# Optimization experiments

Hardware: AMD Instinct MI355X
Metric: run time of the kernel (lower is better)

## Reference

```python
import jax, jax.numpy as jnp
import numpy as np

WINDOW = 512
OVERLAP = 64
STRIDE = WINDOW - OVERLAP  # 448
HEADS = 12
HEAD_DIM = 3072 // HEADS  # 256
SCALE = 1.0 / np.sqrt(HEAD_DIM)


def setup_inputs() -> dict:
    key = jax.random.key(0)
    ks = jax.random.split(key, 9)
    B, S, H = 1, 8192, 3072
    w = 0.02  # weight init scale
    return {
        "hidden_states": jax.random.normal(ks[0], (B, S, H), jnp.float32),
        "Wq": jax.random.normal(ks[1], (H, H), jnp.float32) * w,
        "bq": jnp.zeros((H,), jnp.float32),
        "Wk": jax.random.normal(ks[2], (H, H), jnp.float32) * w,
        "bk": jnp.zeros((H,), jnp.float32),
        "Wv": jax.random.normal(ks[3], (H, H), jnp.float32) * w,
        "bv": jnp.zeros((H,), jnp.float32),
        "Wo": jax.random.normal(ks[4], (H, H), jnp.float32) * w,
        "bo": jnp.zeros((H,), jnp.float32),
    }


def reference(hidden_states, Wq, bq, Wk, bk, Wv, bv, Wo, bo):
    B, S, H = hidden_states.shape
    n_win = -(-S // STRIDE)  # ceil: windows start at 0, STRIDE, 2*STRIDE, ... < S
    starts = np.arange(n_win) * STRIDE                      # static
    idx = starts[:, None] + np.arange(WINDOW)[None, :]      # [n_win, W]
    valid = jnp.asarray(idx < S)                            # [n_win, W] bool
    idx_c = np.minimum(idx, S - 1)                          # clamp for gather

    # Gather overlapping windows: [B, n_win, W, H] (redundant QKV on overlap, as in original)
    win = hidden_states[:, idx_c]

    def proj(Wm, bm):
        y = jnp.einsum('bnwh,oh->bnwo', win, Wm) + bm
        return y.reshape(B, n_win, WINDOW, HEADS, HEAD_DIM)

    q = proj(Wq, bq)
    k = proj(Wk, bk)
    v = proj(Wv, bv)

    scores = jnp.einsum('bnqhd,bnkhd->bnhqk', q, k) * SCALE  # [B,n_win,heads,W,W]
    # Padded (out-of-range) key positions of the short last window must not attend
    scores = jnp.where(valid[None, :, None, None, :], scores, -1e9)
    attn = jax.nn.softmax(scores, axis=-1)
    ctx = jnp.einsum('bnhqk,bnkhd->bnqhd', attn, v)
    ctx = ctx.reshape(B, n_win, WINDOW, H)
    out_w = jnp.einsum('bnwh,oh->bnwo', ctx, Wo) + bo        # [B,n_win,W,H]

    # zero padded query rows, then overlap-add + average
    out_w = out_w * valid[None, :, :, None].astype(out_w.dtype)
    flat_idx = jnp.asarray(idx_c.reshape(-1))                # [n_win*W]
    output = jnp.zeros((B, S, H), out_w.dtype).at[:, flat_idx].add(
        out_w.reshape(B, -1, H))
    counts = jnp.zeros((S,), out_w.dtype).at[flat_idx].add(
        valid.reshape(-1).astype(out_w.dtype))
    return output / jnp.maximum(counts, 1.0)[None, :, None]
```

## Files before the change

kernel.cpp:

```cpp
#include <hip/hip_runtime.h>
#include <hip/hip_bf16.h>
#include <stdint.h>

#define SEQ   8192
#define HDIM  3072
#define NWIN  19
#define WINL  512
#define STR   448
#define NHEAD 12
#define DHEAD 256
#define QKVN  9216
#define ATTN_SCALE 0.0625f

typedef unsigned short u16;
typedef __bf16 bf16x8 __attribute__((ext_vector_type(8)));
typedef float  f32x4  __attribute__((ext_vector_type(4)));
typedef unsigned short us8 __attribute__((ext_vector_type(8)));

__device__ __forceinline__ u16 f2b(float x) {
  return __builtin_bit_cast(u16, __float2bfloat16(x));
}
__device__ __forceinline__ float b2f(u16 u) {
  return __builtin_bit_cast(float, (unsigned int)(u) << 16);
}
__device__ __forceinline__ void gload_lds16(const void* g, void* l) {
  __builtin_amdgcn_global_load_lds(
      (const __attribute__((address_space(1))) void*)g,
      (__attribute__((address_space(3))) void*)l, 16, 0, 0);
}

__global__ __launch_bounds__(256) void cvt_f32_bf16(const float* __restrict__ src,
                                                    u16* __restrict__ dst, int n8) {
  int i = blockIdx.x * 256 + threadIdx.x;
  if (i >= n8) return;
  const float4* s4 = (const float4*)src;
  float4 a = s4[2 * i], b = s4[2 * i + 1];
  us8 o;
  o[0] = f2b(a.x); o[1] = f2b(a.y); o[2] = f2b(a.z); o[3] = f2b(a.w);
  o[4] = f2b(b.x); o[5] = f2b(b.y); o[6] = f2b(b.z); o[7] = f2b(b.w);
  *((us8*)dst + i) = o;
}

__global__ __launch_bounds__(256) void biascat(const float* __restrict__ bq,
                                               const float* __restrict__ bk,
                                               const float* __restrict__ bv,
                                               float* __restrict__ dst) {
  int i = blockIdx.x * 256 + threadIdx.x;
  if (i >= QKVN) return;
  dst[i] = (i < HDIM) ? bq[i] : ((i < 2 * HDIM) ? bk[i - HDIM] : bv[i - 2 * HDIM]);
}

template <bool BF16OUT>
__global__ __launch_bounds__(512, 2) void gemm256(const u16* __restrict__ A,
                                                  const u16* __restrict__ B,
                                                  const float* __restrict__ bias,
                                                  float* __restrict__ outF,
                                                  u16* __restrict__ outB,
                                                  int M, int N, int K, int nbn) {
  __shared__ __align__(16) u16 As[4][4096];
  __shared__ __align__(16) u16 Bs[4][4096];
  const int tid = threadIdx.x;
  const int w = tid >> 6, l = tid & 63;
  const int wm = w >> 2, wn = w & 3;
  const int fr = l & 15, g = l >> 4;
  const int nwg = gridDim.x;
  const int bid = blockIdx.x;
  const int wg = (bid & 7) * (nwg >> 3) + (bid >> 3);
  const int bm = wg / nbn, bn = wg % nbn;

  const u16* Ab = A + (size_t)bm * 256 * K;
  const u16* Bb = B + (size_t)bn * 256 * K;

  const int r_st = w * 16 + (l >> 2);
  const int s_st = ((l & 3) ^ ((l >> 3) & 3)) * 8;
  const int sw = (g ^ ((fr >> 1) & 3)) * 8;

  f32x4 acc[8][4];
#pragma unroll
  for (int i = 0; i < 8; ++i)
#pragma unroll
    for (int j = 0; j < 4; ++j) acc[i][j] = (f32x4){0.f, 0.f, 0.f, 0.f};

  auto stA = [&](int U, int h) {
    gload_lds16(Ab + (size_t)(h * 128 + r_st) * K + U * 32 + s_st,
                (char*)&As[(2 * U + h) & 3][0] + w * 1024);
  };
  auto stB = [&](int U, int h) {
    gload_lds16(Bb + (size_t)(h * 128 + r_st) * K + U * 32 + s_st,
                (char*)&Bs[(2 * U + h) & 3][0] + w * 1024);
  };

  stA(0, 0); stA(0, 1); stB(0, 0); stB(0, 1); stA(1, 0); stA(1, 1);
  asm volatile("s_waitcnt vmcnt(2)" ::: "memory");
  __builtin_amdgcn_s_barrier();
  __builtin_amdgcn_sched_barrier(0);

  const int NT = K >> 5;

  auto step = [&](int T, bool doB, bool doA, int vm) {
    const u16* ap = &As[(2 * T + wm) & 3][0] + fr * 32 + sw;
    const u16* bp = &Bs[(2 * T + (wn >> 1)) & 3][0] + (wn & 1) * 64 * 32 + fr * 32 + sw;
    bf16x8 af[8], bf[4];
#pragma unroll
    for (int mi = 0; mi < 8; ++mi) af[mi] = *(const bf16x8*)(ap + mi * 512);
#pragma unroll
    for (int ni = 0; ni < 4; ++ni) bf[ni] = *(const bf16x8*)(bp + ni * 512);
    if (doB) { stB(T + 1, 0); stB(T + 1, 1); }
    __builtin_amdgcn_s_barrier();
    __builtin_amdgcn_s_setprio(1);
#pragma unroll
    for (int mi = 0; mi < 4; ++mi)
#pragma unroll
      for (int ni = 0; ni < 4; ++ni)
        acc[mi][ni] = __builtin_amdgcn_mfma_f32_16x16x32_bf16(af[mi], bf[ni], acc[mi][ni], 0, 0, 0);
    __builtin_amdgcn_s_setprio(0);
    __builtin_amdgcn_s_barrier();
    if (doA) { stA(T + 2, 0); stA(T + 2, 1); }
    __builtin_amdgcn_s_barrier();
    __builtin_amdgcn_s_setprio(1);
#pragma unroll
    for (int mi = 4; mi < 8; ++mi)
#pragma unroll
      for (int ni = 0; ni < 4; ++ni)
        acc[mi][ni] = __builtin_amdgcn_mfma_f32_16x16x32_bf16(af[mi], bf[ni], acc[mi][ni], 0, 0, 0);
    __builtin_amdgcn_s_setprio(0);
    if (vm == 2) asm volatile("s_waitcnt vmcnt(2)" ::: "memory");
    else if (vm == 0) asm volatile("s_waitcnt vmcnt(0)" ::: "memory");
    __builtin_amdgcn_s_barrier();
    __builtin_amdgcn_sched_barrier(0);
  };

#pragma unroll 2
  for (int T = 0; T < NT - 2; ++T) step(T, true, true, 2);
  step(NT - 2, true, false, 0);
  step(NT - 1, false, false, -1);

#pragma unroll
  for (int ni = 0; ni < 4; ++ni) {
    const int c = bn * 256 + wn * 64 + ni * 16 + fr;
    const float bvv = bias ? bias[c] : 0.0f;
#pragma unroll
    for (int mi = 0; mi < 8; ++mi) {
      const int r0 = bm * 256 + wm * 128 + mi * 16 + g * 4;
#pragma unroll
      for (int jj = 0; jj < 4; ++jj) {
        float v = acc[mi][ni][jj] + bvv;
        if (BF16OUT) outB[(size_t)(r0 + jj) * N + c] = f2b(v);
        else         outF[(size_t)(r0 + jj) * N + c] = v;
      }
    }
  }
}

__global__ __launch_bounds__(256) void vtrans(const u16* __restrict__ QKV,
                                              u16* __restrict__ Vt) {
  __shared__ u16 t[64][72];
  const int tid = threadIdx.x;
  const int s0 = blockIdx.x * 64, c0 = blockIdx.y * 64;
  {
    const int r2 = tid >> 3, cc = (tid & 7) * 8;
#pragma unroll
    for (int p = 0; p < 2; ++p) {
      const int row = r2 + p * 32;
      u16 tmp[8];
      *(uint4*)tmp = *(const uint4*)(QKV + (size_t)(s0 + row) * QKVN + 2 * HDIM + c0 + cc);
#pragma unroll
      for (int j = 0; j < 8; ++j) t[row][cc + j] = tmp[j];
    }
  }
  __syncthreads();
  {
    const int cr2 = tid >> 3, sc = tid & 7;
#pragma unroll
    for (int p = 0; p < 2; ++p) {
      const int c = cr2 + p * 32;
      u16 tmp[8];
#pragma unroll
      for (int j = 0; j < 8; ++j) tmp[j] = t[sc * 8 + j][c];
      *(uint4*)(Vt + (size_t)(c0 + c) * SEQ + s0 + sc * 8) = *(uint4*)tmp;
    }
  }
}

__global__ __launch_bounds__(256, 2) void attn_kernel(const u16* __restrict__ QKV,
                                                      const u16* __restrict__ Vt,
                                                      u16* __restrict__ ctxw) {
  __shared__ __align__(16) u16 Ks[64 * 256];
  __shared__ __align__(16) u16 Vts[256 * 64];
  __shared__ __align__(16) u16 Ps[4][16 * 64];
  const int qb = blockIdx.x, h = blockIdx.y, n = blockIdx.z;
  const int tid = threadIdx.x, w = tid >> 6, l = tid & 63;
  const int g = l >> 4, fr = l & 15;
  const int s0 = n * STR;

  bf16x8 qf[8];
  {
    int sq = s0 + qb * 64 + w * 16 + fr;
    if (sq > SEQ - 1) sq = SEQ - 1;
    const u16* qbase = QKV + (size_t)sq * QKVN + h * DHEAD + g * 8;
#pragma unroll
    for (int dc = 0; dc < 8; ++dc) qf[dc] = *(const bf16x8*)(qbase + dc * 32);
  }
  f32x4 ctx[16];
#pragma unroll
  for (int dn = 0; dn < 16; ++dn) ctx[dn] = (f32x4){0.f, 0.f, 0.f, 0.f};
  float mrow[4] = {-3e38f, -3e38f, -3e38f, -3e38f};
  float lrow[4] = {0.f, 0.f, 0.f, 0.f};

  const int kr_in = l >> 5;
  const int kcp = l & 31;
  const int vr_in = l >> 3;
  const int vcp = l & 7;

  for (int kt = 0; kt < 8; ++kt) {
    const int sb = s0 + kt * 64;
#pragma unroll
    for (int i = 0; i < 8; ++i) {
      const int c = i * 4 + w;
      {
        const int krow = c * 2 + kr_in;
        const int cl = kcp ^ (krow & 31);
        int sk = sb + krow;
        if (sk > SEQ - 1) sk = SEQ - 1;
        gload_lds16(QKV + (size_t)sk * QKVN + HDIM + h * DHEAD + cl * 8, (char*)Ks + c * 1024);
      }
      {
        const int d = c * 8 + vr_in;
        const int cl = vcp ^ (d & 7);
        int sv = sb + cl * 8;
        if (sv > SEQ - 8) sv = SEQ - 8;
        gload_lds16(Vt + (size_t)(h * DHEAD + d) * SEQ + sv, (char*)Vts + c * 1024);
      }
    }
    __syncthreads();

    f32x4 sacc[4];
#pragma unroll
    for (int kn = 0; kn < 4; ++kn) sacc[kn] = (f32x4){0.f, 0.f, 0.f, 0.f};
#pragma unroll
    for (int kn = 0; kn < 4; ++kn) {
      const int krow = kn * 16 + fr;
      const char* krp = (const char*)Ks + krow * 512;
      const int rx = krow & 31;
#pragma unroll
      for (int dc = 0; dc < 8; ++dc) {
        bf16x8 kf = *(const bf16x8*)(krp + (((dc * 4 + g) ^ rx) << 4));
        sacc[kn] = __builtin_amdgcn_mfma_f32_16x16x32_bf16(qf[dc], kf, sacc[kn], 0, 0, 0);
      }
    }
    float mt[4];
#pragma unroll
    for (int kn = 0; kn < 4; ++kn) {
      const bool valid = (sb + kn * 16 + fr) < SEQ;
#pragma unroll
      for (int r = 0; r < 4; ++r) {
        float v = valid ? sacc[kn][r] * ATTN_SCALE : -1e9f;
        sacc[kn][r] = v;
        mt[r] = (kn == 0) ? v : fmaxf(mt[r], v);
      }
    }
#pragma unroll
    for (int r = 0; r < 4; ++r) {
#pragma unroll
      for (int off = 1; off < 16; off <<= 1)
        mt[r] = fmaxf(mt[r], __shfl_xor(mt[r], off, 64));
    }
    float corr[4];
#pragma unroll
    for (int r = 0; r < 4; ++r) {
      float mnew = fmaxf(mrow[r], mt[r]);
      corr[r] = __expf(mrow[r] - mnew);
      mrow[r] = mnew;
    }
    float psum[4] = {0.f, 0.f, 0.f, 0.f};
    char* pw = (char*)&Ps[w][0];
#pragma unroll
    for (int kn = 0; kn < 4; ++kn) {
#pragma unroll
      for (int r = 0; r < 4; ++r) {
        float p = __expf(sacc[kn][r] - mrow[r]);
        psum[r] += p;
        const int q = g * 4 + r;
        *(u16*)(pw + q * 128 + ((2 * (kn * 16 + fr)) ^ ((q & 7) << 4))) = f2b(p);
      }
    }
#pragma unroll
    for (int r = 0; r < 4; ++r) {
#pragma unroll
      for (int off = 1; off < 16; off <<= 1)
        psum[r] += __shfl_xor(psum[r], off, 64);
      lrow[r] = lrow[r] * corr[r] + psum[r];
    }
#pragma unroll
    for (int dn = 0; dn < 16; ++dn)
#pragma unroll
      for (int r = 0; r < 4; ++r) ctx[dn][r] *= corr[r];
    __syncthreads();

    bf16x8 pf[2];
#pragma unroll
    for (int kc = 0; kc < 2; ++kc)
      pf[kc] = *(const bf16x8*)(pw + fr * 128 + ((kc * 64 + g * 16) ^ ((fr & 7) << 4)));
#pragma unroll
    for (int dn = 0; dn < 16; ++dn) {
      const int d = dn * 16 + fr;
      const char* vrp = (const char*)Vts + d * 128;
      const int dx = d & 7;
#pragma unroll
      for (int kc = 0; kc < 2; ++kc) {
        bf16x8 vf = *(const bf16x8*)(vrp + (((kc * 4 + g) ^ dx) << 4));
        ctx[dn] = __builtin_amdgcn_mfma_f32_16x16x32_bf16(pf[kc], vf, ctx[dn], 0, 0, 0);
      }
    }
    __syncthreads();
  }
  float inv[4];
#pragma unroll
  for (int r = 0; r < 4; ++r) inv[r] = 1.0f / lrow[r];
  const int qrow0 = qb * 64 + w * 16 + g * 4;
#pragma unroll
  for (int dn = 0; dn < 16; ++dn) {
#pragma unroll
    for (int r = 0; r < 4; ++r) {
      ctxw[(size_t)(n * WINL + qrow0 + r) * HDIM + h * DHEAD + dn * 16 + fr] =
          f2b(ctx[dn][r] * inv[r]);
    }
  }
}

__global__ __launch_bounds__(256) void combine_kernel(const u16* __restrict__ ctxw,
                                                      u16* __restrict__ ctx_avg) {
  int idx = blockIdx.x * 256 + threadIdx.x;
  if (idx >= SEQ * (HDIM / 8)) return;
  const int s = idx / (HDIM / 8);
  const int cc = (idx % (HDIM / 8)) * 8;
  const int w1 = s / STR;
  const int off1 = s - w1 * STR;
  us8 a = *(const us8*)(ctxw + (size_t)(w1 * WINL + off1) * HDIM + cc);
  if (w1 >= 1 && off1 < (WINL - STR)) {
    us8 b = *(const us8*)(ctxw + (size_t)((w1 - 1) * WINL + off1 + STR) * HDIM + cc);
#pragma unroll
    for (int j = 0; j < 8; ++j) a[j] = f2b(0.5f * (b2f(a[j]) + b2f(b[j])));
  }
  *(us8*)(ctx_avg + (size_t)s * HDIM + cc) = a;
}

__global__ void ws_marker(float* out, float v) { out[0] = v; }

extern "C" void kernel_launch(void* const* d_in, const int* in_sizes, int n_in,
                              void* d_out, int out_size, void* d_ws, size_t ws_size,
                              hipStream_t stream) {
  const float* X  = (const float*)d_in[0];
  const float* Wq = (const float*)d_in[1];
  const float* bq = (const float*)d_in[2];
  const float* Wk = (const float*)d_in[3];
  const float* bk = (const float*)d_in[4];
  const float* Wv = (const float*)d_in[5];
  const float* bv = (const float*)d_in[6];
  const float* Wo = (const float*)d_in[7];
  const float* bo = (const float*)d_in[8];
  float* out = (float*)d_out;

  const size_t OFF_XB   = 0;
  const size_t OFF_WQKV = 50331648;
  const size_t OFF_WO   = 106954752;
  const size_t OFF_QKV  = 125829120;
  const size_t OFF_VT   = 276824064;
  const size_t OFF_BIAS = 327155712;
  const size_t WS_NEED  = 327192576;
  if (ws_size < WS_NEED) {
    hipMemsetAsync(d_out, 0, (size_t)out_size * 4, stream);
    ws_marker<<<1, 1, 0, stream>>>(out, (float)(ws_size / 1048576));
    return;
  }
  char* ws = (char*)d_ws;
  u16* Xb      = (u16*)(ws + OFF_XB);
  u16* Wqkvb   = (u16*)(ws + OFF_WQKV);
  u16* Wob     = (u16*)(ws + OFF_WO);
  u16* QKV     = (u16*)(ws + OFF_QKV);
  u16* Vt      = (u16*)(ws + OFF_VT);
  float* biasQ = (float*)(ws + OFF_BIAS);
  u16* ctxw    = (u16*)d_out;
  u16* ctx_avg = Xb;

  cvt_f32_bf16<<<12288, 256, 0, stream>>>(X, Xb, SEQ * HDIM / 8);
  cvt_f32_bf16<<<4608, 256, 0, stream>>>(Wq, Wqkvb, HDIM * HDIM / 8);
  cvt_f32_bf16<<<4608, 256, 0, stream>>>(Wk, Wqkvb + (size_t)HDIM * HDIM, HDIM * HDIM / 8);
  cvt_f32_bf16<<<4608, 256, 0, stream>>>(Wv, Wqkvb + (size_t)2 * HDIM * HDIM, HDIM * HDIM / 8);
  cvt_f32_bf16<<<4608, 256, 0, stream>>>(Wo, Wob, HDIM * HDIM / 8);
  biascat<<<36, 256, 0, stream>>>(bq, bk, bv, biasQ);

  gemm256<true><<<dim3((SEQ / 256) * (QKVN / 256)), 512, 0, stream>>>(
      Xb, Wqkvb, biasQ, nullptr, QKV, SEQ, QKVN, HDIM, QKVN / 256);

  vtrans<<<dim3(SEQ / 64, HDIM / 64), 256, 0, stream>>>(QKV, Vt);

  attn_kernel<<<dim3(8, NHEAD, NWIN), 256, 0, stream>>>(QKV, Vt, ctxw);

  combine_kernel<<<12288, 256, 0, stream>>>(ctxw, ctx_avg);

  gemm256<false><<<dim3((SEQ / 256) * (HDIM / 256)), 512, 0, stream>>>(
      ctx_avg, Wob, bo, out, nullptr, SEQ, HDIM, HDIM, HDIM / 256);
}
```

Measured before the change: 994.0 us.

## Deepen GEMM prefetch to three K-stages and remap tiles per XCD

```diff
diff --git a/kernel.cpp b/kernel.cpp
--- a/kernel.cpp
+++ b/kernel.cpp
@@ -56,17 +56,15 @@
                                                   const float* __restrict__ bias,
                                                   float* __restrict__ outF,
                                                   u16* __restrict__ outB,
-                                                  int M, int N, int K, int nbn) {
-  __shared__ __align__(16) u16 As[4][4096];
-  __shared__ __align__(16) u16 Bs[4][4096];
+                                                  int N, int K) {
+  __shared__ __align__(16) u16 As[4][8192];
+  __shared__ __align__(16) u16 Bs[4][8192];
   const int tid = threadIdx.x;
   const int w = tid >> 6, l = tid & 63;
   const int wm = w >> 2, wn = w & 3;
   const int fr = l & 15, g = l >> 4;
-  const int nwg = gridDim.x;
-  const int bid = blockIdx.x;
-  const int wg = (bid & 7) * (nwg >> 3) + (bid >> 3);
-  const int bm = wg / nbn, bn = wg % nbn;
+  const int xcd = blockIdx.x & 7, loc = blockIdx.x >> 3;
+  const int bn = loc >> 2, bm = xcd * 4 + (loc & 3);
 
   const u16* Ab = A + (size_t)bm * 256 * K;
   const u16* Bb = B + (size_t)bn * 256 * K;
@@ -81,32 +79,39 @@
 #pragma unroll
     for (int j = 0; j < 4; ++j) acc[i][j] = (f32x4){0.f, 0.f, 0.f, 0.f};
 
-  auto stA = [&](int U, int h) {
-    gload_lds16(Ab + (size_t)(h * 128 + r_st) * K + U * 32 + s_st,
-                (char*)&As[(2 * U + h) & 3][0] + w * 1024);
+  auto stA = [&](int T) {
+    const int s = T & 3;
+#pragma unroll
+    for (int h = 0; h < 2; ++h)
+      gload_lds16(Ab + (size_t)(h * 128 + r_st) * K + T * 32 + s_st,
+                  (char*)&As[s][0] + h * 8192 + w * 1024 + l * 16);
   };
-  auto stB = [&](int U, int h) {
-    gload_lds16(Bb + (size_t)(h * 128 + r_st) * K + U * 32 + s_st,
-                (char*)&Bs[(2 * U + h) & 3][0] + w * 1024);
+  auto stB = [&](int T) {
+    const int s = T & 3;
+#pragma unroll
+    for (int h = 0; h < 2; ++h)
+      gload_lds16(Bb + (size_t)(h * 128 + r_st) * K + T * 32 + s_st,
+                  (char*)&Bs[s][0] + h * 8192 + w * 1024 + l * 16);
   };
 
-  stA(0, 0); stA(0, 1); stB(0, 0); stB(0, 1); stA(1, 0); stA(1, 1);
-  asm volatile("s_waitcnt vmcnt(2)" ::: "memory");
+  stA(0); stB(0); stA(1); stB(1); stA(2); stB(2);
+  asm volatile("s_waitcnt vmcnt(8)" ::: "memory");
   __builtin_amdgcn_s_barrier();
   __builtin_amdgcn_sched_barrier(0);
 
   const int NT = K >> 5;
 
-  auto step = [&](int T, bool doB, bool doA, int vm) {
-    const u16* ap = &As[(2 * T + wm) & 3][0] + fr * 32 + sw;
-    const u16* bp = &Bs[(2 * T + (wn >> 1)) & 3][0] + (wn & 1) * 64 * 32 + fr * 32 + sw;
+  auto step = [&](int T, bool doStage, int vm) {
+    const u16* as_ = &As[T & 3][0] + (wm * 128 + fr) * 32 + sw;
+    const u16* bs_ = &Bs[T & 3][0] + (wn * 64 + fr) * 32 + sw;
     bf16x8 af[8], bf[4];
 #pragma unroll
-    for (int mi = 0; mi < 8; ++mi) af[mi] = *(const bf16x8*)(ap + mi * 512);
-#pragma unroll
-    for (int ni = 0; ni < 4; ++ni) bf[ni] = *(const bf16x8*)(bp + ni * 512);
-    if (doB) { stB(T + 1, 0); stB(T + 1, 1); }
+    for (int mi = 0; mi < 4; ++mi) af[mi] = *(const bf16x8*)(as_ + mi * 512);
+#pragma unroll
+    for (int ni = 0; ni < 4; ++ni) bf[ni] = *(const bf16x8*)(bs_ + ni * 512);
+    if (doStage) stA(T + 3);
     __builtin_amdgcn_s_barrier();
+    asm volatile("s_waitcnt lgkmcnt(0)" ::: "memory");
     __builtin_amdgcn_s_setprio(1);
 #pragma unroll
     for (int mi = 0; mi < 4; ++mi)
@@ -115,8 +120,11 @@
         acc[mi][ni] = __builtin_amdgcn_mfma_f32_16x16x32_bf16(af[mi], bf[ni], acc[mi][ni], 0, 0, 0);
     __builtin_amdgcn_s_setprio(0);
     __builtin_amdgcn_s_barrier();
-    if (doA) { stA(T + 2, 0); stA(T + 2, 1); }
+#pragma unroll
+    for (int mi = 4; mi < 8; ++mi) af[mi] = *(const bf16x8*)(as_ + mi * 512);
+    if (doStage) stB(T + 3);
     __builtin_amdgcn_s_barrier();
+    asm volatile("s_waitcnt lgkmcnt(0)" ::: "memory");
     __builtin_amdgcn_s_setprio(1);
 #pragma unroll
     for (int mi = 4; mi < 8; ++mi)
@@ -124,16 +132,17 @@
       for (int ni = 0; ni < 4; ++ni)
         acc[mi][ni] = __builtin_amdgcn_mfma_f32_16x16x32_bf16(af[mi], bf[ni], acc[mi][ni], 0, 0, 0);
     __builtin_amdgcn_s_setprio(0);
-    if (vm == 2) asm volatile("s_waitcnt vmcnt(2)" ::: "memory");
+    if (vm == 8) asm volatile("s_waitcnt vmcnt(8)" ::: "memory");
+    else if (vm == 4) asm volatile("s_waitcnt vmcnt(4)" ::: "memory");
     else if (vm == 0) asm volatile("s_waitcnt vmcnt(0)" ::: "memory");
     __builtin_amdgcn_s_barrier();
     __builtin_amdgcn_sched_barrier(0);
   };
 
-#pragma unroll 2
-  for (int T = 0; T < NT - 2; ++T) step(T, true, true, 2);
-  step(NT - 2, true, false, 0);
-  step(NT - 1, false, false, -1);
+  for (int T = 0; T < NT - 3; ++T) step(T, true, 8);
+  step(NT - 3, false, 4);
+  step(NT - 2, false, 0);
+  step(NT - 1, false, -1);
 
 #pragma unroll
   for (int ni = 0; ni < 4; ++ni) {
@@ -391,7 +400,7 @@
   biascat<<<36, 256, 0, stream>>>(bq, bk, bv, biasQ);
 
   gemm256<true><<<dim3((SEQ / 256) * (QKVN / 256)), 512, 0, stream>>>(
-      Xb, Wqkvb, biasQ, nullptr, QKV, SEQ, QKVN, HDIM, QKVN / 256);
+      Xb, Wqkvb, biasQ, nullptr, QKV, QKVN, HDIM);
 
   vtrans<<<dim3(SEQ / 64, HDIM / 64), 256, 0, stream>>>(QKV, Vt);
 
@@ -400,5 +409,5 @@
   combine_kernel<<<12288, 256, 0, stream>>>(ctxw, ctx_avg);
 
   gemm256<false><<<dim3((SEQ / 256) * (HDIM / 256)), 512, 0, stream>>>(
-      ctx_avg, Wob, bo, out, nullptr, SEQ, HDIM, HDIM, HDIM / 256);
-}
+      ctx_avg, Wob, bo, out, nullptr, HDIM, HDIM);
+}
```

Measured after the change: 951.2 us. 4.3% less time.
